# Optimization experiments

Measured on AMD Instinct MI355X. Metric: run time of the kernel, lower is better.

Reference implementation:

```python
import jax, jax.numpy as jnp
import numpy as np

DIM = 256
HEADS = 8
WS = 16      # window size
WN = 16      # num windows (img 64x64)
KS = 3
B = 16
IMG = 64


def setup_inputs() -> dict:
    key = jax.random.key(0)
    ks = jax.random.split(key, 12)
    d = DIM
    hid = d // 16  # SE hidden (d >= 64)
    inp = {
        "x": jax.random.normal(ks[0], (B, d, IMG, IMG), dtype=jnp.float32),
        "conv_w": jax.random.normal(ks[1], (WN, d, d, KS, KS), dtype=jnp.float32) * 0.02,
        "wqkv": jax.random.normal(ks[2], (d, 3 * d), dtype=jnp.float32) * 0.02,
        "bqkv": jax.random.normal(ks[3], (3 * d,), dtype=jnp.float32) * 0.02,
        "wout": jax.random.normal(ks[4], (d, d), dtype=jnp.float32) * 0.02,
        "bout": jax.random.normal(ks[5], (d,), dtype=jnp.float32) * 0.02,
        "se_w1": jax.random.normal(ks[6], (WN, hid, d), dtype=jnp.float32) * 0.05,
        "se_b1": jax.random.normal(ks[7], (WN, hid), dtype=jnp.float32) * 0.02,
        "se_w2": jax.random.normal(ks[8], (WN, d, hid), dtype=jnp.float32) * 0.05,
        "se_b2": jax.random.normal(ks[9], (WN, d), dtype=jnp.float32) * 0.02,
        "ln_g": jnp.ones((d,), dtype=jnp.float32),
        "ln_b": jnp.zeros((d,), dtype=jnp.float32),
    }
    return inp


def reference(x, conv_w, wqkv, bqkv, wout, bout, se_w1, se_b1, se_w2, se_b2, ln_g, ln_b):
    Bn, C, H, W = x.shape
    hd = C // HEADS
    scale = hd ** (-0.5)

    # window partition: (WN, B, C, WS, WS), windows in (h_idx, w_idx) row-major order
    xw = x.reshape(Bn, C, H // WS, WS, W // WS, WS).transpose(2, 4, 0, 1, 3, 5)
    xw = xw.reshape(WN, Bn, C, WS, WS)

    # kernel tokens: per-layer weight.view(B, C, -1).permute(0,2,1), cat on axis 1
    last = C * KS * KS // Bn
    kt = conv_w.reshape(WN, Bn, C, last).transpose(1, 0, 3, 2).reshape(Bn, WN * last, C)

    # self-attention over kernel tokens (batch axis becomes dim C after reshape)
    qkv = kt @ wqkv + bqkv                                    # (B, WN*last, 3C)
    qkv = qkv.reshape(C, WN * KS * KS, 3, HEADS, hd).transpose(2, 0, 3, 1, 4)
    q, k, v = qkv[0] * scale, qkv[1], qkv[2]                  # (C, H, T, hd), T = WN*KS*KS
    attn = jax.nn.softmax(jnp.einsum('dhqe,dhke->dhqk', q, k), axis=-1)
    o = jnp.einsum('dhqk,dhke->dhqe', attn, v)
    o = o.transpose(0, 2, 1, 3).reshape(C, WN * KS * KS, C)
    o = o @ wout + bout
    kern = o.reshape(C, WN, KS, KS, C).transpose(1, 0, 4, 2, 3)  # (WN, Cout, Cin, KS, KS)

    # SE gating per window: kernels[i] treated as (batch=C, channels=C, KS, KS)
    pooled = kern.mean(axis=(3, 4))                            # (WN, C, C)
    h = jax.nn.relu(jnp.einsum('wbc,whc->wbh', pooled, se_w1) + se_b1[:, None, :])
    s = jax.nn.sigmoid(jnp.einsum('wbh,wch->wbc', h, se_w2) + se_b2[:, None, :])
    kern = kern * s[:, :, :, None, None]

    # per-window conv as a single grouped conv (groups = WN)
    xg = xw.transpose(1, 0, 2, 3, 4).reshape(Bn, WN * C, WS, WS)
    wg = kern.reshape(WN * C, C, KS, KS)
    yg = jax.lax.conv_general_dilated(xg, wg, (1, 1), ((1, 1), (1, 1)),
                                      feature_group_count=WN)
    yw = yg.reshape(Bn, WN, C, WS, WS).transpose(1, 0, 2, 3, 4)  # (WN, B, C, WS, WS)

    # window reverse
    y = yw.reshape(H // WS, W // WS, Bn, C, WS, WS).transpose(2, 3, 0, 4, 1, 5)
    y = y.reshape(Bn, C, H, W)

    # channel layernorm (eps=1e-5) + residual
    yn = y.transpose(0, 2, 3, 1)
    mu = yn.mean(-1, keepdims=True)
    var = ((yn - mu) ** 2).mean(-1, keepdims=True)
    yn = (yn - mu) / jnp.sqrt(var + 1e-5) * ln_g + ln_b
    return x + yn.transpose(0, 3, 1, 2)
```

## Files before the change

kernel.cpp:

```cpp
#include <hip/hip_runtime.h>

typedef __bf16 bf16;
typedef __bf16 bf16x8 __attribute__((ext_vector_type(8)));
typedef _Float16 f16;
typedef _Float16 f16x8 __attribute__((ext_vector_type(8)));
typedef float f32x4 __attribute__((ext_vector_type(4)));

#define SCALE_Q 0.17677669529663687f
#define KSCALE 64.0f
#define KSCALE_INV 0.015625f

__global__ __launch_bounds__(256) void k_prep_w(const float* __restrict__ wqkv,
                                                const float* __restrict__ wout,
                                                bf16* __restrict__ wqkv_t,
                                                f16* __restrict__ wout_h,
                                                f16* __restrict__ wout_l) {
    int n = blockIdx.x, k = threadIdx.x;
    if (n < 768) {
        wqkv_t[n * 256 + k] = (bf16)wqkv[k * 768 + n];
    } else {
        float f = wout[k * 256 + (n - 768)] * KSCALE;
        f16 hi = (f16)f;
        wout_h[(n - 768) * 256 + k] = hi;
        wout_l[(n - 768) * 256 + k] = (f16)(f - (float)hi);
    }
}

__global__ __launch_bounds__(256) void k_build_kt(const float* __restrict__ conv_w,
                                                  bf16* __restrict__ kt) {
    __shared__ float lds[2304];
    int w = blockIdx.x >> 8, co = blockIdx.x & 255;
    const float* src = conv_w + (size_t)(w * 256 + co) * 2304;
    for (int i = threadIdx.x; i < 2304; i += 256) lds[i] = src[i];
    __syncthreads();
    int b = co >> 4, c0 = (co & 15) << 4;
    size_t rbase = (size_t)(b * 16 + w) * 144;
    for (int i = threadIdx.x; i < 2304; i += 256) {
        int t = i >> 4, m = i & 15;
        kt[(rbase + t) * 256 + c0 + m] = (bf16)lds[m * 144 + t];
    }
}

typedef const __attribute__((address_space(1))) unsigned int* gas_t;
typedef __attribute__((address_space(3))) unsigned int* las_t;

__device__ __forceinline__ void async_copy16(const void* g, void* l) {
    __builtin_amdgcn_global_load_lds((gas_t)g, (las_t)l, 16, 0, 0);
}

__device__ __forceinline__ void stage_tile_async(const void* __restrict__ gsrc_, int ld,
                                                 void* lds_) {
    const unsigned short* gsrc = (const unsigned short*)gsrc_;
    unsigned short* lds_tile = (unsigned short*)lds_;
    int t = threadIdx.x;
    int wave = t >> 6, lane = t & 63;
#pragma unroll
    for (int c = 0; c < 2; c++) {
        int chunk = wave * 2 + c;
        int row = chunk * 16 + (lane >> 2);
        int p = (lane & 3) ^ (row & 3);
        async_copy16(gsrc + (size_t)row * ld + (p << 3), lds_tile + chunk * 512);
    }
}

__device__ __forceinline__ void mfma_tile_bf16(const bf16* As, const bf16* Bs,
                                               f32x4 acc[4][4]) {
    int lane = threadIdx.x & 63;
    int wave = threadIdx.x >> 6;
    int wm = (wave >> 1) * 64, wn = (wave & 1) * 64;
    int lrow = lane & 15, quad = lane >> 4;
    bf16x8 af[4], bfr[4];
#pragma unroll
    for (int i = 0; i < 4; i++) {
        int r = wm + i * 16 + lrow;
        af[i] = *(const bf16x8*)(As + r * 32 + ((quad ^ (r & 3)) << 3));
        int n = wn + i * 16 + lrow;
        bfr[i] = *(const bf16x8*)(Bs + n * 32 + ((quad ^ (n & 3)) << 3));
    }
#pragma unroll
    for (int i = 0; i < 4; i++)
#pragma unroll
        for (int j = 0; j < 4; j++)
            acc[i][j] = __builtin_amdgcn_mfma_f32_16x16x32_bf16(af[i], bfr[j], acc[i][j], 0, 0, 0);
}

__device__ __forceinline__ void mfma_tile_f16_dual(const f16* As, const f16* Bhs,
                                                   const f16* Bls, f32x4 acc[4][4]) {
    int lane = threadIdx.x & 63;
    int wave = threadIdx.x >> 6;
    int wm = (wave >> 1) * 64, wn = (wave & 1) * 64;
    int lrow = lane & 15, quad = lane >> 4;
    f16x8 af[4], bh[4], bl[4];
#pragma unroll
    for (int i = 0; i < 4; i++) {
        int r = wm + i * 16 + lrow;
        af[i] = *(const f16x8*)(As + r * 32 + ((quad ^ (r & 3)) << 3));
        int n = wn + i * 16 + lrow;
        bh[i] = *(const f16x8*)(Bhs + n * 32 + ((quad ^ (n & 3)) << 3));
        bl[i] = *(const f16x8*)(Bls + n * 32 + ((quad ^ (n & 3)) << 3));
    }
#pragma unroll
    for (int i = 0; i < 4; i++)
#pragma unroll
        for (int j = 0; j < 4; j++) {
            acc[i][j] = __builtin_amdgcn_mfma_f32_16x16x32_f16(af[i], bh[j], acc[i][j], 0, 0, 0);
            acc[i][j] = __builtin_amdgcn_mfma_f32_16x16x32_f16(af[i], bl[j], acc[i][j], 0, 0, 0);
        }
}

__global__ __launch_bounds__(256) void k_gemm_qkv(const bf16* __restrict__ A,
                                                  const bf16* __restrict__ Bt,
                                                  const float* __restrict__ bias,
                                                  bf16* __restrict__ outb,
                                                  int N, int K) {
    __shared__ __align__(16) bf16 As[128 * 32];
    __shared__ __align__(16) bf16 Bs[128 * 32];
    int m0 = blockIdx.y * 128, n0 = blockIdx.x * 128;
    f32x4 acc[4][4] = {};
    for (int k0 = 0; k0 < K; k0 += 32) {
        stage_tile_async(A + (size_t)m0 * K + k0, K, As);
        stage_tile_async(Bt + (size_t)n0 * K + k0, K, Bs);
        __syncthreads();
        mfma_tile_bf16(As, Bs, acc);
        __syncthreads();
    }
    int lane = threadIdx.x & 63, wave = threadIdx.x >> 6;
    int wm = (wave >> 1) * 64, wn = (wave & 1) * 64;
    int lrow = lane & 15, quad = lane >> 4;
#pragma unroll
    for (int i = 0; i < 4; i++)
#pragma unroll
        for (int j = 0; j < 4; j++) {
            int col = n0 + wn + j * 16 + lrow;
            float bv = bias[col];
#pragma unroll
            for (int rr = 0; rr < 4; rr++) {
                int row = m0 + wm + i * 16 + quad * 4 + rr;
                float v = acc[i][j][rr] + bv;
                if (col < 256) v *= SCALE_Q;
                outb[(size_t)row * N + col] = (bf16)v;
            }
        }
}

__global__ __launch_bounds__(256) void k_gemm_split2(const f16* __restrict__ Ag,
                                                     const f16* __restrict__ Bhg,
                                                     const f16* __restrict__ Blg,
                                                     const float* __restrict__ bias,
                                                     float* __restrict__ outf,
                                                     int N, int K) {
    __shared__ __align__(16) f16 As[128 * 32];
    __shared__ __align__(16) f16 Bh[128 * 32];
    __shared__ __align__(16) f16 Bl[128 * 32];
    int m0 = blockIdx.y * 128, n0 = blockIdx.x * 128;
    f32x4 acc[4][4] = {};
    for (int k0 = 0; k0 < K; k0 += 32) {
        stage_tile_async(Ag + (size_t)m0 * K + k0, K, As);
        stage_tile_async(Bhg + (size_t)n0 * K + k0, K, Bh);
        stage_tile_async(Blg + (size_t)n0 * K + k0, K, Bl);
        __syncthreads();
        mfma_tile_f16_dual(As, Bh, Bl, acc);
        __syncthreads();
    }
    int lane = threadIdx.x & 63, wave = threadIdx.x >> 6;
    int wm = (wave >> 1) * 64, wn = (wave & 1) * 64;
    int lrow = lane & 15, quad = lane >> 4;
#pragma unroll
    for (int i = 0; i < 4; i++)
#pragma unroll
        for (int j = 0; j < 4; j++) {
            int col = n0 + wn + j * 16 + lrow;
            float bv = bias[col];
#pragma unroll
            for (int rr = 0; rr < 4; rr++) {
                int row = m0 + wm + i * 16 + quad * 4 + rr;
                outf[(size_t)row * N + col] = acc[i][j][rr] * KSCALE_INV + bv;
            }
        }
}

__global__ __launch_bounds__(256) void k_attn(const bf16* __restrict__ qkv,
                                              f16* __restrict__ o16) {
    __shared__ bf16 Qs[144 * 32];
    __shared__ bf16 Ks[144 * 32];
    __shared__ f16 Vt[32 * 160];
    __shared__ f16 Ps[4 * 16 * 168];
    int d = blockIdx.x >> 3, h = blockIdx.x & 7;
    const bf16* base = qkv + (size_t)d * 144 * 768 + h * 32;
    int t = threadIdx.x;

    for (int i = t; i < 512; i += 256) Vt[(i >> 4) * 160 + 144 + (i & 15)] = (f16)0.f;
    for (int i = t; i < 576; i += 256) {
        int row = i >> 2, part = i & 3;
        const bf16* rp = base + (size_t)row * 768;
        uint4 vq = *(const uint4*)(rp + (part << 3));
        uint4 vk = *(const uint4*)(rp + 256 + (part << 3));
        int sw = ((part ^ (row & 3)) << 3);
        *(uint4*)(Qs + row * 32 + sw) = vq;
        *(uint4*)(Ks + row * 32 + sw) = vk;
        bf16x8 v8 = *(const bf16x8*)(rp + 512 + (part << 3));
#pragma unroll
        for (int j = 0; j < 8; j++) Vt[(part * 8 + j) * 160 + row] = (f16)(float)v8[j];
    }
    __syncthreads();

    int wave = t >> 6, lane = t & 63;
    int lrow = lane & 15, quad = lane >> 4;
    f16* Pw = Ps + wave * 16 * 168;
    for (int i = lane; i < 256; i += 64) Pw[(i >> 4) * 168 + 144 + (i & 15)] = (f16)0.f;

    bf16x8 kf[9];
#pragma unroll
    for (int nt = 0; nt < 9; nt++) {
        int r = nt * 16 + lrow;
        kf[nt] = *(const bf16x8*)(Ks + r * 32 + ((quad ^ (r & 3)) << 3));
    }

    for (int mt = wave; mt < 9; mt += 4) {
        int qr = mt * 16 + lrow;
        bf16x8 qf = *(const bf16x8*)(Qs + qr * 32 + ((quad ^ (qr & 3)) << 3));
        f32x4 s[9];
#pragma unroll
        for (int nt = 0; nt < 9; nt++) {
            f32x4 z = {0.f, 0.f, 0.f, 0.f};
            s[nt] = __builtin_amdgcn_mfma_f32_16x16x32_bf16(qf, kf[nt], z, 0, 0, 0);
        }
        f32x4 mx = s[0];
#pragma unroll
        for (int nt = 1; nt < 9; nt++)
#pragma unroll
            for (int c = 0; c < 4; c++) mx[c] = fmaxf(mx[c], s[nt][c]);
#pragma unroll
        for (int off = 1; off < 16; off <<= 1)
#pragma unroll
            for (int c = 0; c < 4; c++) mx[c] = fmaxf(mx[c], __shfl_xor(mx[c], off));
        f32x4 sm = {0.f, 0.f, 0.f, 0.f};
#pragma unroll
        for (int nt = 0; nt < 9; nt++)
#pragma unroll
            for (int c = 0; c < 4; c++) {
                float e = __expf(s[nt][c] - mx[c]);
                s[nt][c] = e;
                sm[c] += e;
            }
#pragma unroll
        for (int off = 1; off < 16; off <<= 1)
#pragma unroll
            for (int c = 0; c < 4; c++) sm[c] += __shfl_xor(sm[c], off);
        f32x4 inv;
#pragma unroll
        for (int c = 0; c < 4; c++) inv[c] = 1.f / sm[c];
#pragma unroll
        for (int nt = 0; nt < 9; nt++)
#pragma unroll
            for (int c = 0; c < 4; c++)
                Pw[(quad * 4 + c) * 168 + nt * 16 + lrow] = (f16)(s[nt][c] * inv[c]);

        f32x4 o0 = {0.f, 0.f, 0.f, 0.f}, o1 = {0.f, 0.f, 0.f, 0.f};
#pragma unroll
        for (int kt = 0; kt < 5; kt++) {
            f16x8 pf = *(const f16x8*)(Pw + lrow * 168 + kt * 32 + quad * 8);
            f16x8 v0 = *(const f16x8*)(Vt + lrow * 160 + kt * 32 + quad * 8);
            f16x8 v1 = *(const f16x8*)(Vt + (16 + lrow) * 160 + kt * 32 + quad * 8);
            o0 = __builtin_amdgcn_mfma_f32_16x16x32_f16(pf, v0, o0, 0, 0, 0);
            o1 = __builtin_amdgcn_mfma_f32_16x16x32_f16(pf, v1, o1, 0, 0, 0);
        }
        size_t ro = ((size_t)d * 144 + mt * 16) * 256 + h * 32;
#pragma unroll
        for (int c = 0; c < 4; c++) {
            size_t rr = ro + (size_t)(quad * 4 + c) * 256;
            o16[rr + lrow] = (f16)o0[c];
            o16[rr + 16 + lrow] = (f16)o1[c];
        }
    }
}

__global__ __launch_bounds__(256) void k_se_scale(const float* __restrict__ kern,
                                                  const float* __restrict__ w1,
                                                  const float* __restrict__ b1,
                                                  const float* __restrict__ w2,
                                                  const float* __restrict__ b2,
                                                  f16* __restrict__ kern_hi,
                                                  f16* __restrict__ kern_lo) {
    __shared__ float pooled[256];
    __shared__ float hbuf[16];
    int w = blockIdx.x >> 8, Co = blockIdx.x & 255;
    int ci = threadIdx.x;
    const float* kb = kern + (size_t)(Co * 16 + w) * 9 * 256;
    float pv = 0.f;
#pragma unroll
    for (int k9 = 0; k9 < 9; k9++) pv += kb[k9 * 256 + ci];
    pooled[ci] = pv * (1.f / 9.f);
    __syncthreads();
    if (ci < 16) {
        const float* w1p = w1 + (size_t)(w * 16 + ci) * 256;
        float hs = b1[w * 16 + ci];
        for (int c = 0; c < 256; c++) hs += pooled[c] * w1p[c];
        hbuf[ci] = fmaxf(hs, 0.f);
    }
    __syncthreads();
    const float* w2p = w2 + (size_t)(w * 256 + ci) * 16;
    float ss = b2[w * 256 + ci];
#pragma unroll
    for (int j = 0; j < 16; j++) ss += hbuf[j] * w2p[j];
    float s = (1.f / (1.f + __expf(-ss))) * KSCALE;
    size_t outo = (size_t)(w * 256 + Co) * 2304;
    f16* khi = kern_hi + outo;
    f16* klo = kern_lo + outo;
#pragma unroll
    for (int k9 = 0; k9 < 9; k9++) {
        float f = kb[k9 * 256 + ci] * s;
        f16 hi = (f16)f;
        khi[k9 * 256 + ci] = hi;
        klo[k9 * 256 + ci] = (f16)(f - (float)hi);
    }
}

__global__ __launch_bounds__(256) void k_zero(uint4* __restrict__ p, int n4) {
    int stride = gridDim.x * 256;
    for (int i = blockIdx.x * 256 + threadIdx.x; i < n4; i += stride)
        p[i] = uint4{0u, 0u, 0u, 0u};
}

__global__ __launch_bounds__(256) void k_fill_xcl(const float* __restrict__ x,
                                                  f16* __restrict__ xcl) {
    int bx = blockIdx.x;
    int b = bx >> 6, gy = bx & 63;
    int wrow = gy >> 4, py = gy & 15;
    int ci = threadIdx.x;
    const float* xp = x + ((size_t)(b * 256 + ci) * 64 + gy) * 64;
    for (int wx = 0; wx < 4; wx++) {
        int w = wrow * 4 + wx;
        size_t o = (((size_t)(w * 16 + b) * 18 + py + 1) * 18 + 1) * 256 + ci;
#pragma unroll
        for (int px = 0; px < 16; px++)
            xcl[o + (size_t)px * 256] = (f16)xp[wx * 16 + px];
    }
}

__global__ __launch_bounds__(256) void k_conv_gemm(const f16* __restrict__ xcl,
                                                   const f16* __restrict__ kern_hi,
                                                   const f16* __restrict__ kern_lo,
                                                   float* __restrict__ y) {
    __shared__ __align__(16) f16 As[128 * 32];
    __shared__ __align__(16) f16 Bh[128 * 32];
    __shared__ __align__(16) f16 Bl[128 * 32];
    int w = blockIdx.z;
    int m0 = blockIdx.y * 128, n0 = blockIdx.x * 128;
    const f16* xw = xcl + (size_t)w * 16 * 18 * 18 * 256;
    const f16* Bth = kern_hi + (size_t)w * 256 * 2304;
    const f16* Btl = kern_lo + (size_t)w * 256 * 2304;
    f32x4 acc[4][4] = {};
    int t = threadIdx.x;
    int wave = t >> 6, lane = t & 63;
    for (int k0 = 0; k0 < 2304; k0 += 32) {
        int k9 = k0 >> 8, ci0 = k0 & 255;
        int dy = k9 / 3, dx = k9 % 3;
#pragma unroll
        for (int c = 0; c < 2; c++) {
            int chunk = wave * 2 + c;
            int row = chunk * 16 + (lane >> 2);
            int p = (lane & 3) ^ (row & 3);
            int m = m0 + row;
            int b = m >> 8, pp = m & 255, py = pp >> 4, px = pp & 15;
            size_t go = ((size_t)(b * 18 + py + dy) * 18 + px + dx) * 256 + ci0 + (p << 3);
            async_copy16(xw + go, As + chunk * 512);
        }
        stage_tile_async(Bth + (size_t)n0 * 2304 + k0, 2304, Bh);
        stage_tile_async(Btl + (size_t)n0 * 2304 + k0, 2304, Bl);
        __syncthreads();
        mfma_tile_f16_dual(As, Bh, Bl, acc);
        __syncthreads();
    }
    int lrow = lane & 15, quad = lane >> 4;
    int wm = (wave >> 1) * 64, wn = (wave & 1) * 64;
    float* yw = y + (size_t)w * 4096 * 256;
#pragma unroll
    for (int i = 0; i < 4; i++)
#pragma unroll
        for (int j = 0; j < 4; j++) {
            int col = n0 + wn + j * 16 + lrow;
#pragma unroll
            for (int rr = 0; rr < 4; rr++) {
                int row = m0 + wm + i * 16 + quad * 4 + rr;
                yw[(size_t)row * 256 + col] = acc[i][j][rr] * KSCALE_INV;
            }
        }
}

__global__ __launch_bounds__(256) void k_ln_res(const float* __restrict__ y,
                                                const float* __restrict__ x,
                                                const float* __restrict__ g,
                                                const float* __restrict__ be,
                                                float* __restrict__ out) {
    int bx = blockIdx.x;
    int b = bx >> 6, gy = bx & 63;
    int t = threadIdx.x;
    int j = t >> 2, sub = t & 3;
    int w = (gy >> 4) * 4 + (j >> 4);
    int p = (gy & 15) * 16 + (j & 15);
    const float* yp = y + ((size_t)w * 4096 + b * 256 + p) * 256 + sub * 64;
    float vals[64];
    float sum = 0.f, sq = 0.f;
#pragma unroll
    for (int c = 0; c < 64; c++) {
        float v = yp[c];
        vals[c] = v;
        sum += v; sq += v * v;
    }
    sum += __shfl_xor(sum, 1); sq += __shfl_xor(sq, 1);
    sum += __shfl_xor(sum, 2); sq += __shfl_xor(sq, 2);
    float mean = sum * (1.f / 256.f);
    float var = sq * (1.f / 256.f) - mean * mean;
    float rstd = rsqrtf(var + 1e-5f);
    const float* xp = x + ((size_t)(b * 256 + sub * 64) * 64 + gy) * 64 + j;
    float* op = out + ((size_t)(b * 256 + sub * 64) * 64 + gy) * 64 + j;
#pragma unroll
    for (int c = 0; c < 64; c++) {
        int cc = sub * 64 + c;
        op[(size_t)c * 4096] = (vals[c] - mean) * rstd * g[cc] + be[cc] + xp[(size_t)c * 4096];
    }
}

extern "C" void kernel_launch(void* const* d_in, const int* in_sizes, int n_in,
                              void* d_out, int out_size, void* d_ws, size_t ws_size,
                              hipStream_t stream) {
    const float* x      = (const float*)d_in[0];
    const float* conv_w = (const float*)d_in[1];
    const float* wqkv   = (const float*)d_in[2];
    const float* bqkv   = (const float*)d_in[3];
    const float* wout   = (const float*)d_in[4];
    const float* bout   = (const float*)d_in[5];
    const float* se_w1  = (const float*)d_in[6];
    const float* se_b1  = (const float*)d_in[7];
    const float* se_w2  = (const float*)d_in[8];
    const float* se_b2  = (const float*)d_in[9];
    const float* ln_g   = (const float*)d_in[10];
    const float* ln_b   = (const float*)d_in[11];
    float* out = (float*)d_out;

    char* ws = (char*)d_ws;
    bf16*  kt      = (bf16*)(ws + 0);
    f16*   o16     = (f16*)(ws + 0);
    f16*   kern_hi = (f16*)(ws + 0);
    f16*   kern_lo = (f16*)(ws + 18874368);
    bf16*  wqkv_t  = (bf16*)(ws + 37748736);
    f16*   wout_h  = (f16*)(ws + 38141952);
    f16*   wout_l  = (f16*)(ws + 38273024);
    f16*   xcl     = (f16*)(ws + 38404096);
    bf16*  qkv     = (bf16*)(ws + 80871424);
    float* kern_f  = (float*)(ws + 80871424);
    float* y       = (float*)(ws + 80871424);

    k_prep_w<<<1024, 256, 0, stream>>>(wqkv, wout, wqkv_t, wout_h, wout_l);
    k_build_kt<<<4096, 256, 0, stream>>>(conv_w, kt);
    k_gemm_qkv<<<dim3(6, 288), 256, 0, stream>>>(kt, wqkv_t, bqkv, qkv, 768, 256);
    k_attn<<<2048, 256, 0, stream>>>(qkv, o16);
    k_gemm_split2<<<dim3(2, 288), 256, 0, stream>>>(o16, wout_h, wout_l, bout, kern_f, 256, 256);
    k_se_scale<<<4096, 256, 0, stream>>>(kern_f, se_w1, se_b1, se_w2, se_b2, kern_hi, kern_lo);
    k_zero<<<2048, 256, 0, stream>>>((uint4*)xcl, 42467328 / 16);
    k_fill_xcl<<<1024, 256, 0, stream>>>(x, xcl);
    k_conv_gemm<<<dim3(2, 32, 16), 256, 0, stream>>>(xcl, kern_hi, kern_lo, y);
    k_ln_res<<<1024, 256, 0, stream>>>(y, x, ln_g, ln_b, out);
}
```

Measured before the change: 553.8 us.

## Double-buffer LDS tiles with async prefetch and change swizzle in GEMM kernels

Converts the three MFMA GEMM kernels (qkv, split2 output projection, and the windowed conv GEMM) from single-buffered load-then-compute loops to double-buffered pipelines. The next K-tile is prefetched with global_load_lds while the current tile is multiplied, using explicit vmcnt waits and raw barriers. Per-thread global offsets are precomputed outside the loop, and the LDS XOR swizzle now uses (row>>1)&3 to reduce bank conflicts on fragment reads. This doubles LDS usage per block, which may lower occupancy, and relies on hand-written waitcnt ordering being correct.

```diff
diff --git a/kernel.cpp b/kernel.cpp
--- a/kernel.cpp
+++ b/kernel.cpp
@@ -48,21 +48,6 @@
     __builtin_amdgcn_global_load_lds((gas_t)g, (las_t)l, 16, 0, 0);
 }
 
-__device__ __forceinline__ void stage_tile_async(const void* __restrict__ gsrc_, int ld,
-                                                 void* lds_) {
-    const unsigned short* gsrc = (const unsigned short*)gsrc_;
-    unsigned short* lds_tile = (unsigned short*)lds_;
-    int t = threadIdx.x;
-    int wave = t >> 6, lane = t & 63;
-#pragma unroll
-    for (int c = 0; c < 2; c++) {
-        int chunk = wave * 2 + c;
-        int row = chunk * 16 + (lane >> 2);
-        int p = (lane & 3) ^ (row & 3);
-        async_copy16(gsrc + (size_t)row * ld + (p << 3), lds_tile + chunk * 512);
-    }
-}
-
 __device__ __forceinline__ void mfma_tile_bf16(const bf16* As, const bf16* Bs,
                                                f32x4 acc[4][4]) {
     int lane = threadIdx.x & 63;
@@ -73,9 +58,9 @@
 #pragma unroll
     for (int i = 0; i < 4; i++) {
         int r = wm + i * 16 + lrow;
-        af[i] = *(const bf16x8*)(As + r * 32 + ((quad ^ (r & 3)) << 3));
+        af[i] = *(const bf16x8*)(As + r * 32 + ((quad ^ ((r >> 1) & 3)) << 3));
         int n = wn + i * 16 + lrow;
-        bfr[i] = *(const bf16x8*)(Bs + n * 32 + ((quad ^ (n & 3)) << 3));
+        bfr[i] = *(const bf16x8*)(Bs + n * 32 + ((quad ^ ((n >> 1) & 3)) << 3));
     }
 #pragma unroll
     for (int i = 0; i < 4; i++)
@@ -94,10 +79,10 @@
 #pragma unroll
     for (int i = 0; i < 4; i++) {
         int r = wm + i * 16 + lrow;
-        af[i] = *(const f16x8*)(As + r * 32 + ((quad ^ (r & 3)) << 3));
+        af[i] = *(const f16x8*)(As + r * 32 + ((quad ^ ((r >> 1) & 3)) << 3));
         int n = wn + i * 16 + lrow;
-        bh[i] = *(const f16x8*)(Bhs + n * 32 + ((quad ^ (n & 3)) << 3));
-        bl[i] = *(const f16x8*)(Bls + n * 32 + ((quad ^ (n & 3)) << 3));
+        bh[i] = *(const f16x8*)(Bhs + n * 32 + ((quad ^ ((n >> 1) & 3)) << 3));
+        bl[i] = *(const f16x8*)(Bls + n * 32 + ((quad ^ ((n >> 1) & 3)) << 3));
     }
 #pragma unroll
     for (int i = 0; i < 4; i++)
@@ -113,18 +98,40 @@
                                                   const float* __restrict__ bias,
                                                   bf16* __restrict__ outb,
                                                   int N, int K) {
-    __shared__ __align__(16) bf16 As[128 * 32];
-    __shared__ __align__(16) bf16 Bs[128 * 32];
+    __shared__ __align__(16) bf16 As[2][128 * 32];
+    __shared__ __align__(16) bf16 Bs[2][128 * 32];
     int m0 = blockIdx.y * 128, n0 = blockIdx.x * 128;
+    int t = threadIdx.x, wave = t >> 6, lane = t & 63;
+    int chunk0 = wave * 2, chunk1 = chunk0 + 1;
+    int row0 = chunk0 * 16 + (lane >> 2), row1 = row0 + 16;
+    int sw = ((lane & 3) ^ ((row0 >> 1) & 3)) << 3;
+    const unsigned short* Ag = (const unsigned short*)A;
+    const unsigned short* Bg = (const unsigned short*)Bt;
+    size_t a0 = (size_t)(m0 + row0) * K + sw, a1 = (size_t)(m0 + row1) * K + sw;
+    size_t b0 = (size_t)(n0 + row0) * K + sw, b1 = (size_t)(n0 + row1) * K + sw;
     f32x4 acc[4][4] = {};
-    for (int k0 = 0; k0 < K; k0 += 32) {
-        stage_tile_async(A + (size_t)m0 * K + k0, K, As);
-        stage_tile_async(Bt + (size_t)n0 * K + k0, K, Bs);
-        __syncthreads();
-        mfma_tile_bf16(As, Bs, acc);
-        __syncthreads();
-    }
-    int lane = threadIdx.x & 63, wave = threadIdx.x >> 6;
+#define STG_QKV(cur, k0)                                        \
+    async_copy16(Ag + a0 + (k0), &As[cur][chunk0 * 512]);       \
+    async_copy16(Ag + a1 + (k0), &As[cur][chunk1 * 512]);       \
+    async_copy16(Bg + b0 + (k0), &Bs[cur][chunk0 * 512]);       \
+    async_copy16(Bg + b1 + (k0), &Bs[cur][chunk1 * 512]);
+    STG_QKV(0, 0);
+    int cur = 0, NT = K >> 5;
+#pragma unroll 1
+    for (int it = 0; it < NT; it++) {
+        if (it < NT - 1) {
+            STG_QKV(cur ^ 1, (it + 1) << 5);
+            asm volatile("s_waitcnt vmcnt(4)" ::: "memory");
+        } else {
+            asm volatile("s_waitcnt vmcnt(0)" ::: "memory");
+        }
+        __builtin_amdgcn_s_barrier();
+        mfma_tile_bf16(As[cur], Bs[cur], acc);
+        asm volatile("s_waitcnt lgkmcnt(0)" ::: "memory");
+        __builtin_amdgcn_s_barrier();
+        cur ^= 1;
+    }
+#undef STG_QKV
     int wm = (wave >> 1) * 64, wn = (wave & 1) * 64;
     int lrow = lane & 15, quad = lane >> 4;
 #pragma unroll
@@ -143,26 +150,50 @@
         }
 }
 
-__global__ __launch_bounds__(256) void k_gemm_split2(const f16* __restrict__ Ag,
+__global__ __launch_bounds__(256) void k_gemm_split2(const f16* __restrict__ Ag_,
                                                      const f16* __restrict__ Bhg,
                                                      const f16* __restrict__ Blg,
                                                      const float* __restrict__ bias,
                                                      float* __restrict__ outf,
                                                      int N, int K) {
-    __shared__ __align__(16) f16 As[128 * 32];
-    __shared__ __align__(16) f16 Bh[128 * 32];
-    __shared__ __align__(16) f16 Bl[128 * 32];
+    __shared__ __align__(16) f16 As[2][128 * 32];
+    __shared__ __align__(16) f16 Bh[2][128 * 32];
+    __shared__ __align__(16) f16 Bl[2][128 * 32];
     int m0 = blockIdx.y * 128, n0 = blockIdx.x * 128;
+    int t = threadIdx.x, wave = t >> 6, lane = t & 63;
+    int chunk0 = wave * 2, chunk1 = chunk0 + 1;
+    int row0 = chunk0 * 16 + (lane >> 2), row1 = row0 + 16;
+    int sw = ((lane & 3) ^ ((row0 >> 1) & 3)) << 3;
+    const unsigned short* Au = (const unsigned short*)Ag_;
+    const unsigned short* Bhu = (const unsigned short*)Bhg;
+    const unsigned short* Blu = (const unsigned short*)Blg;
+    size_t a0 = (size_t)(m0 + row0) * K + sw, a1 = (size_t)(m0 + row1) * K + sw;
+    size_t b0 = (size_t)(n0 + row0) * K + sw, b1 = (size_t)(n0 + row1) * K + sw;
     f32x4 acc[4][4] = {};
-    for (int k0 = 0; k0 < K; k0 += 32) {
-        stage_tile_async(Ag + (size_t)m0 * K + k0, K, As);
-        stage_tile_async(Bhg + (size_t)n0 * K + k0, K, Bh);
-        stage_tile_async(Blg + (size_t)n0 * K + k0, K, Bl);
-        __syncthreads();
-        mfma_tile_f16_dual(As, Bh, Bl, acc);
-        __syncthreads();
-    }
-    int lane = threadIdx.x & 63, wave = threadIdx.x >> 6;
+#define STG_SP2(cur, k0)                                        \
+    async_copy16(Au + a0 + (k0), &As[cur][chunk0 * 512]);       \
+    async_copy16(Au + a1 + (k0), &As[cur][chunk1 * 512]);       \
+    async_copy16(Bhu + b0 + (k0), &Bh[cur][chunk0 * 512]);      \
+    async_copy16(Bhu + b1 + (k0), &Bh[cur][chunk1 * 512]);      \
+    async_copy16(Blu + b0 + (k0), &Bl[cur][chunk0 * 512]);      \
+    async_copy16(Blu + b1 + (k0), &Bl[cur][chunk1 * 512]);
+    STG_SP2(0, 0);
+    int cur = 0, NT = K >> 5;
+#pragma unroll 1
+    for (int it = 0; it < NT; it++) {
+        if (it < NT - 1) {
+            STG_SP2(cur ^ 1, (it + 1) << 5);
+            asm volatile("s_waitcnt vmcnt(6)" ::: "memory");
+        } else {
+            asm volatile("s_waitcnt vmcnt(0)" ::: "memory");
+        }
+        __builtin_amdgcn_s_barrier();
+        mfma_tile_f16_dual(As[cur], Bh[cur], Bl[cur], acc);
+        asm volatile("s_waitcnt lgkmcnt(0)" ::: "memory");
+        __builtin_amdgcn_s_barrier();
+        cur ^= 1;
+    }
+#undef STG_SP2
     int wm = (wave >> 1) * 64, wn = (wave & 1) * 64;
     int lrow = lane & 15, quad = lane >> 4;
 #pragma unroll
@@ -342,36 +373,54 @@
                                                    const f16* __restrict__ kern_hi,
                                                    const f16* __restrict__ kern_lo,
                                                    float* __restrict__ y) {
-    __shared__ __align__(16) f16 As[128 * 32];
-    __shared__ __align__(16) f16 Bh[128 * 32];
-    __shared__ __align__(16) f16 Bl[128 * 32];
+    __shared__ __align__(16) f16 As[2][128 * 32];
+    __shared__ __align__(16) f16 Bh[2][128 * 32];
+    __shared__ __align__(16) f16 Bl[2][128 * 32];
     int w = blockIdx.z;
     int m0 = blockIdx.y * 128, n0 = blockIdx.x * 128;
-    const f16* xw = xcl + (size_t)w * 16 * 18 * 18 * 256;
-    const f16* Bth = kern_hi + (size_t)w * 256 * 2304;
-    const f16* Btl = kern_lo + (size_t)w * 256 * 2304;
+    const unsigned short* xw = (const unsigned short*)(xcl + (size_t)w * 16 * 18 * 18 * 256);
+    const unsigned short* Bthu = (const unsigned short*)(kern_hi + (size_t)w * 256 * 2304);
+    const unsigned short* Btlu = (const unsigned short*)(kern_lo + (size_t)w * 256 * 2304);
+    int t = threadIdx.x, wave = t >> 6, lane = t & 63;
+    int chunk0 = wave * 2, chunk1 = chunk0 + 1;
+    int row0 = chunk0 * 16 + (lane >> 2), row1 = row0 + 16;
+    int sw = ((lane & 3) ^ ((row0 >> 1) & 3)) << 3;
+    int mA0 = m0 + row0, mA1 = m0 + row1;
+    int bA0 = mA0 >> 8, pp0 = mA0 & 255;
+    int bA1 = mA1 >> 8, pp1 = mA1 & 255;
+    size_t aA0 = ((size_t)(bA0 * 18 + (pp0 >> 4)) * 18 + (pp0 & 15)) * 256 + sw;
+    size_t aA1 = ((size_t)(bA1 * 18 + (pp1 >> 4)) * 18 + (pp1 & 15)) * 256 + sw;
+    size_t bB0 = (size_t)(n0 + row0) * 2304 + sw;
+    size_t bB1 = (size_t)(n0 + row1) * 2304 + sw;
     f32x4 acc[4][4] = {};
-    int t = threadIdx.x;
-    int wave = t >> 6, lane = t & 63;
-    for (int k0 = 0; k0 < 2304; k0 += 32) {
-        int k9 = k0 >> 8, ci0 = k0 & 255;
-        int dy = k9 / 3, dx = k9 % 3;
-#pragma unroll
-        for (int c = 0; c < 2; c++) {
-            int chunk = wave * 2 + c;
-            int row = chunk * 16 + (lane >> 2);
-            int p = (lane & 3) ^ (row & 3);
-            int m = m0 + row;
-            int b = m >> 8, pp = m & 255, py = pp >> 4, px = pp & 15;
-            size_t go = ((size_t)(b * 18 + py + dy) * 18 + px + dx) * 256 + ci0 + (p << 3);
-            async_copy16(xw + go, As + chunk * 512);
-        }
-        stage_tile_async(Bth + (size_t)n0 * 2304 + k0, 2304, Bh);
-        stage_tile_async(Btl + (size_t)n0 * 2304 + k0, 2304, Bl);
-        __syncthreads();
-        mfma_tile_f16_dual(As, Bh, Bl, acc);
-        __syncthreads();
-    }
+#define STG_CONV(cur, k0)                                                      \
+    {                                                                          \
+        int k9_ = (k0) >> 8;                                                   \
+        int koff_ = ((k9_ / 3) * 18 + (k9_ % 3)) * 256 + ((k0) & 255);         \
+        async_copy16(xw + aA0 + koff_, &As[cur][chunk0 * 512]);                \
+        async_copy16(xw + aA1 + koff_, &As[cur][chunk1 * 512]);                \
+        async_copy16(Bthu + bB0 + (k0), &Bh[cur][chunk0 * 512]);               \
+        async_copy16(Bthu + bB1 + (k0), &Bh[cur][chunk1 * 512]);               \
+        async_copy16(Btlu + bB0 + (k0), &Bl[cur][chunk0 * 512]);               \
+        async_copy16(Btlu + bB1 + (k0), &Bl[cur][chunk1 * 512]);               \
+    }
+    STG_CONV(0, 0);
+    int cur = 0;
+#pragma unroll 1
+    for (int it = 0; it < 72; it++) {
+        if (it < 71) {
+            STG_CONV(cur ^ 1, (it + 1) << 5);
+            asm volatile("s_waitcnt vmcnt(6)" ::: "memory");
+        } else {
+            asm volatile("s_waitcnt vmcnt(0)" ::: "memory");
+        }
+        __builtin_amdgcn_s_barrier();
+        mfma_tile_f16_dual(As[cur], Bh[cur], Bl[cur], acc);
+        asm volatile("s_waitcnt lgkmcnt(0)" ::: "memory");
+        __builtin_amdgcn_s_barrier();
+        cur ^= 1;
+    }
+#undef STG_CONV
     int lrow = lane & 15, quad = lane >> 4;
     int wm = (wave >> 1) * 64, wn = (wave & 1) * 64;
     float* yw = y + (size_t)w * 4096 * 256;
```

After: 535.1 us. 1.04x faster.
